# Kernel tuning notes

Hardware: AMD Instinct MI355X
Metric: run time of the kernel (lower is better)

Reference implementation:

```python
import jax, jax.numpy as jnp
import numpy as np

B, N, WIDTH, HEADS = 4, 2048, 1024, 16
HEAD_DIM = WIDTH // HEADS  # 64


def setup_inputs() -> dict:
    key = jax.random.key(0)
    k1, k2, k3 = jax.random.split(key, 3)
    x = jax.random.normal(k1, (B, N, WIDTH), dtype=jnp.float32)
    # Linear weights stored as [in, out] (torch stores [out, in]; math y = x @ W_in_out + b)
    w_qkv = jax.random.normal(k2, (WIDTH, 3 * WIDTH), dtype=jnp.float32) * (1.0 / np.sqrt(WIDTH))
    b_qkv = jnp.zeros((3 * WIDTH,), dtype=jnp.float32)
    w_proj = jax.random.normal(k3, (WIDTH, WIDTH), dtype=jnp.float32) * (1.0 / np.sqrt(WIDTH))
    b_proj = jnp.zeros((WIDTH,), dtype=jnp.float32)
    return {"x": x, "w_qkv": w_qkv, "b_qkv": b_qkv, "w_proj": w_proj, "b_proj": b_proj}


def reference(x, w_qkv, b_qkv, w_proj, b_proj):
    bs, n_ctx, width = x.shape
    qkv = x @ w_qkv + b_qkv                      # [b, n, 3*width]
    attn_ch = HEAD_DIM                            # width // heads
    scale = 1.0 / np.sqrt(np.sqrt(attn_ch))       # 1/sqrt(sqrt(d)) applied to q and k
    qkv = qkv.reshape(bs, n_ctx, HEADS, 3 * attn_ch)
    q, k, v = jnp.split(qkv, 3, axis=-1)          # each [b, n, h, d]
    weight = jnp.einsum('bthc,bshc->bhts', q * scale, k * scale)
    weight = jax.nn.softmax(weight, axis=-1)
    out = jnp.einsum('bhts,bshc->bthc', weight, v).reshape(bs, n_ctx, -1)
    return out @ w_proj + b_proj
```

## Files before the change

kernel.cpp:

```cpp
#include <hip/hip_runtime.h>

typedef __attribute__((ext_vector_type(8))) short bf16x8;
typedef __attribute__((ext_vector_type(4))) float f32x4;
typedef __attribute__((ext_vector_type(8))) unsigned short u16x8;
typedef __attribute__((ext_vector_type(4))) unsigned short u16x4;
typedef __attribute__((ext_vector_type(2))) unsigned u32x2;

__device__ __forceinline__ unsigned short f2bf(float f) {
  unsigned u = __builtin_bit_cast(unsigned, f);
  return (unsigned short)((u + 0x7fffu + ((u >> 16) & 1u)) >> 16);
}

__device__ __forceinline__ unsigned cvt_pk_bf16(float lo, float hi) {
  unsigned r;
  asm("v_cvt_pk_bf16_f32 %0, %1, %2" : "=v"(r) : "v"(lo), "v"(hi));
  return r;
}

__device__ __forceinline__ void gl_lds16(const void* g, void* l) {
  __builtin_amdgcn_global_load_lds((const __attribute__((address_space(1))) unsigned*)g,
                                   (__attribute__((address_space(3))) unsigned*)l, 16, 0, 0);
}

__global__ __launch_bounds__(256) void k_prep(const float* __restrict__ x,
                                              unsigned short* __restrict__ xb,
                                              const float* __restrict__ wq,
                                              unsigned short* __restrict__ wqT,
                                              const float* __restrict__ wp,
                                              unsigned short* __restrict__ wpT) {
  __shared__ float tile[32][33];
  const int bx = blockIdx.x;
  const int t = threadIdx.x;
  if (bx < 4096) {
    const int i = bx * 256 + t;
    const float4* s = (const float4*)x;
    float4 a = s[2 * i], b = s[2 * i + 1];
    u16x8 o;
    o[0] = f2bf(a.x); o[1] = f2bf(a.y); o[2] = f2bf(a.z); o[3] = f2bf(a.w);
    o[4] = f2bf(b.x); o[5] = f2bf(b.y); o[6] = f2bf(b.z); o[7] = f2bf(b.w);
    *(u16x8*)(xb + 8 * (size_t)i) = o;
    return;
  }
  const int b = bx - 4096;
  const float* w;
  unsigned short* wT;
  int Nn, bb;
  if (b < 3072) { w = wq; wT = wqT; Nn = 3072; bb = b; }
  else          { w = wp; wT = wpT; Nn = 1024; bb = b - 3072; }
  const int k0 = (bb & 31) * 32, n0 = (bb >> 5) * 32;
  const int i = t >> 3, j = (t & 7) * 4;
  float4 v = *(const float4*)(w + (size_t)(k0 + i) * Nn + n0 + j);
  tile[i][j] = v.x; tile[i][j + 1] = v.y; tile[i][j + 2] = v.z; tile[i][j + 3] = v.w;
  __syncthreads();
  const int n = i, k4 = j;
  u16x4 o;
  o[0] = f2bf(tile[k4 + 0][n]); o[1] = f2bf(tile[k4 + 1][n]);
  o[2] = f2bf(tile[k4 + 2][n]); o[3] = f2bf(tile[k4 + 3][n]);
  *(u16x4*)(wT + (size_t)(n0 + n) * 1024 + k0 + k4) = o;
}

template <int EPI>
__global__ __launch_bounds__(256) void k_gemm(const unsigned short* __restrict__ A,
                                              const unsigned short* __restrict__ Bt,
                                              const float* __restrict__ bias, int Nx,
                                              float* __restrict__ outF,
                                              unsigned short* __restrict__ Qb,
                                              unsigned short* __restrict__ Kb,
                                              unsigned short* __restrict__ Vb) {
  __shared__ __attribute__((aligned(16))) unsigned short As[3][128 * 32];
  __shared__ __attribute__((aligned(16))) unsigned short Bs[3][128 * 32];
  const int t = threadIdx.x;
  const int jj = blockIdx.x >> 3;
  const int brow = ((blockIdx.x & 7) * 8 + (jj & 7)) * 128;
  const int bcol = (jj >> 3) * 128;
  const int lane = t & 63, wid = t >> 6;
  const int wr = (wid >> 1) * 64, wc = (wid & 1) * 64;
  const int g = lane >> 4, qr = lane & 15;
  const f32x4 fzero = {0.f, 0.f, 0.f, 0.f};
  f32x4 acc[4][4];
#pragma unroll
  for (int i = 0; i < 4; ++i)
#pragma unroll
    for (int n = 0; n < 4; ++n) acc[i][n] = fzero;
  const int srow = t >> 2;
  const int sg = (t & 3) ^ (srow & 3);
  const unsigned short* Ag0 = A + (size_t)(brow + srow) * 1024 + sg * 8;
  const unsigned short* Bg0 = Bt + (size_t)(bcol + srow) * 1024 + sg * 8;

#define STAGE(s_, kt_)                                        \
  do {                                                        \
    const int koff = (kt_) * 32;                              \
    gl_lds16(Ag0 + koff, &As[s_][t * 8]);                     \
    gl_lds16(Ag0 + 64 * 1024 + koff, &As[s_][2048 + t * 8]);  \
    gl_lds16(Bg0 + koff, &Bs[s_][t * 8]);                     \
    gl_lds16(Bg0 + 64 * 1024 + koff, &Bs[s_][2048 + t * 8]);  \
  } while (0)

  STAGE(0, 0);
  STAGE(1, 1);
  for (int kt = 0; kt < 32; ++kt) {
    const int s = kt % 3;
    if (kt < 31) {
      asm volatile("s_waitcnt vmcnt(4)" ::: "memory");
    } else {
      asm volatile("s_waitcnt vmcnt(0)" ::: "memory");
    }
    __builtin_amdgcn_s_barrier();
    __builtin_amdgcn_sched_barrier(0);
    bf16x8 a[4], b[4];
#pragma unroll
    for (int i = 0; i < 4; ++i) {
      const int r = wr + i * 16 + qr;
      a[i] = *(const bf16x8*)&As[s][r * 32 + ((g ^ (r & 3)) << 3)];
    }
#pragma unroll
    for (int n = 0; n < 4; ++n) {
      const int r = wc + n * 16 + qr;
      b[n] = *(const bf16x8*)&Bs[s][r * 32 + ((g ^ (r & 3)) << 3)];
    }
    __builtin_amdgcn_s_setprio(1);
#pragma unroll
    for (int i = 0; i < 4; ++i)
#pragma unroll
      for (int n = 0; n < 4; ++n)
        acc[i][n] = __builtin_amdgcn_mfma_f32_16x16x32_bf16(a[i], b[n], acc[i][n], 0, 0, 0);
    __builtin_amdgcn_s_setprio(0);
    if (kt < 30) STAGE((kt + 2) % 3, kt + 2);
  }
#undef STAGE
#pragma unroll
  for (int i = 0; i < 4; ++i) {
#pragma unroll
    for (int n = 0; n < 4; ++n) {
      const int col = bcol + wc + n * 16 + qr;
      const float bv = bias[col];
      float v4[4];
#pragma unroll
      for (int r = 0; r < 4; ++r) v4[r] = acc[i][n][r] + bv;
      const int row0 = brow + wr + i * 16 + g * 4;
      if constexpr (EPI == 0) {
#pragma unroll
        for (int r = 0; r < 4; ++r) outF[(size_t)(row0 + r) * Nx + col] = v4[r];
      } else {
        const int bb = row0 >> 11, tkn0 = row0 & 2047;
        const unsigned c = (unsigned)col;
        const unsigned h = c / 192u;
        const unsigned rem = c - h * 192u;
        const unsigned which = rem >> 6, d = rem & 63u;
        if (which == 2u) {
          u16x4 pk;
#pragma unroll
          for (int r = 0; r < 4; ++r) pk[r] = f2bf(v4[r]);
          *(u16x4*)&Vb[(size_t)(((unsigned)bb * 16u + h) * 64u + d) * 2048u + (unsigned)tkn0] = pk;
        } else {
          const float sc = (which == 0u) ? (0.35355339059327373f * 1.4426950408889634f)
                                         : 0.35355339059327373f;
          unsigned short* dst = (which == 0u) ? Qb : Kb;
#pragma unroll
          for (int r = 0; r < 4; ++r)
            dst[(size_t)(((unsigned)bb * 16u + h) * 2048u + (unsigned)(tkn0 + r)) * 64u + d] =
                f2bf(v4[r] * sc);
        }
      }
    }
  }
}

__global__ __launch_bounds__(512, 4) void k_attn(const unsigned short* __restrict__ Qb,
                                                 const unsigned short* __restrict__ Kb,
                                                 const unsigned short* __restrict__ Vt,
                                                 unsigned short* __restrict__ Ao) {
  __shared__ __attribute__((aligned(16))) unsigned short Kl[2][64][64];
  __shared__ __attribute__((aligned(16))) unsigned short Vl[2][64][64];
  __shared__ __attribute__((aligned(16))) unsigned short Pl[8][2][16][72];
  const int bid = blockIdx.x;
  const int bh = (bid & 7) * 8 + ((bid >> 3) & 7);
  const int qt = bid >> 6;
  const int t = threadIdx.x, lane = t & 63, w = t >> 6;
  const int g = lane >> 4, q = lane & 15;
  const int q0 = qt * 256 + w * 32;
  const unsigned short* Qbase = Qb + ((size_t)bh * 2048 + q0) * 64;
  const char* Kg = (const char*)(Kb + (size_t)bh * 2048 * 64);
  const char* Vg = (const char*)(Vt + (size_t)bh * 64 * 2048);
  const int lr = lane >> 3, lc = lane & 7;
  const int swz = (lc ^ lr) << 4;
  const char* Ksrc = Kg + (size_t)(8 * w + lr) * 128 + swz;
  const char* Vsrc = Vg + (size_t)(8 * w + lr) * 4096 + swz;
  unsigned short* Kd[2], *Vd[2];
  Kd[0] = &Kl[0][8 * w][0] + lane * 8;
  Kd[1] = &Kl[1][8 * w][0] + lane * 8;
  Vd[0] = &Vl[0][8 * w][0] + lane * 8;
  Vd[1] = &Vl[1][8 * w][0] + lane * 8;

#define STAGE(buf, it_)                              \
  do {                                               \
    gl_lds16(Ksrc + (size_t)(it_) * 8192, Kd[buf]);  \
    gl_lds16(Vsrc + (size_t)(it_) * 128, Vd[buf]);   \
  } while (0)

  bf16x8 qf[2][2];
#pragma unroll
  for (int G = 0; G < 2; ++G)
#pragma unroll
    for (int h = 0; h < 2; ++h)
      qf[G][h] = *(const bf16x8*)(Qbase + (size_t)(G * 16 + q) * 64 + h * 32 + g * 8);
  const f32x4 fzero = {0.f, 0.f, 0.f, 0.f};
  f32x4 o0[4], o1[4];
#pragma unroll
  for (int i = 0; i < 4; ++i) { o0[i] = fzero; o1[i] = fzero; }
  float l0 = 0.f, l1 = 0.f;

  STAGE(0, 0);
  __syncthreads();

  for (int it = 0; it < 32; ++it) {
    const int cur = it & 1;
    if (it < 31) STAGE(cur ^ 1, it + 1);
    f32x4 s0[4], s1[4];
    __builtin_amdgcn_s_setprio(1);
#pragma unroll
    for (int kf = 0; kf < 4; ++kf) {
      const int row = kf * 16 + q;
      const char* kp = (const char*)&Kl[cur][row][0];
      const int sw = (row & 7) << 4;
      bf16x8 kaL = *(const bf16x8*)(kp + ((g * 16) ^ sw));
      bf16x8 kaH = *(const bf16x8*)(kp + ((64 + g * 16) ^ sw));
      s0[kf] = __builtin_amdgcn_mfma_f32_16x16x32_bf16(kaL, qf[0][0], fzero, 0, 0, 0);
      s0[kf] = __builtin_amdgcn_mfma_f32_16x16x32_bf16(kaH, qf[0][1], s0[kf], 0, 0, 0);
      s1[kf] = __builtin_amdgcn_mfma_f32_16x16x32_bf16(kaL, qf[1][0], fzero, 0, 0, 0);
      s1[kf] = __builtin_amdgcn_mfma_f32_16x16x32_bf16(kaH, qf[1][1], s1[kf], 0, 0, 0);
    }
    __builtin_amdgcn_s_setprio(0);
    {
      unsigned short* Pw = &Pl[w][0][q][0];
#pragma unroll
      for (int kf = 0; kf < 4; ++kf) {
        const float e0 = __builtin_amdgcn_exp2f(s0[kf][0]);
        const float e1 = __builtin_amdgcn_exp2f(s0[kf][1]);
        const float e2 = __builtin_amdgcn_exp2f(s0[kf][2]);
        const float e3 = __builtin_amdgcn_exp2f(s0[kf][3]);
        l0 += (e0 + e1) + (e2 + e3);
        u32x2 pk;
        pk[0] = cvt_pk_bf16(e0, e1);
        pk[1] = cvt_pk_bf16(e2, e3);
        *(u32x2*)(Pw + (8 * kf + 2 * g) * 2) = pk;
      }
    }
    {
      unsigned short* Pw = &Pl[w][1][q][0];
#pragma unroll
      for (int kf = 0; kf < 4; ++kf) {
        const float e0 = __builtin_amdgcn_exp2f(s1[kf][0]);
        const float e1 = __builtin_amdgcn_exp2f(s1[kf][1]);
        const float e2 = __builtin_amdgcn_exp2f(s1[kf][2]);
        const float e3 = __builtin_amdgcn_exp2f(s1[kf][3]);
        l1 += (e0 + e1) + (e2 + e3);
        u32x2 pk;
        pk[0] = cvt_pk_bf16(e0, e1);
        pk[1] = cvt_pk_bf16(e2, e3);
        *(u32x2*)(Pw + (8 * kf + 2 * g) * 2) = pk;
      }
    }
    asm volatile("" ::: "memory");
    const bf16x8 pa00 = *(const bf16x8*)&Pl[w][0][q][g * 8];
    const bf16x8 pa01 = *(const bf16x8*)&Pl[w][0][q][32 + g * 8];
    const bf16x8 pa10 = *(const bf16x8*)&Pl[w][1][q][g * 8];
    const bf16x8 pa11 = *(const bf16x8*)&Pl[w][1][q][32 + g * 8];
    __builtin_amdgcn_s_setprio(1);
#pragma unroll
    for (int dblk = 0; dblk < 4; ++dblk) {
      const int row = dblk * 16 + q;
      const char* vp = (const char*)&Vl[cur][row][0];
      const int sw = (row & 7) << 4;
      bf16x8 vL = *(const bf16x8*)(vp + ((g * 16) ^ sw));
      bf16x8 vH = *(const bf16x8*)(vp + ((64 + g * 16) ^ sw));
      o0[dblk] = __builtin_amdgcn_mfma_f32_16x16x32_bf16(vL, pa00, o0[dblk], 0, 0, 0);
      o0[dblk] = __builtin_amdgcn_mfma_f32_16x16x32_bf16(vH, pa01, o0[dblk], 0, 0, 0);
      o1[dblk] = __builtin_amdgcn_mfma_f32_16x16x32_bf16(vL, pa10, o1[dblk], 0, 0, 0);
      o1[dblk] = __builtin_amdgcn_mfma_f32_16x16x32_bf16(vH, pa11, o1[dblk], 0, 0, 0);
    }
    __builtin_amdgcn_s_setprio(0);
    __syncthreads();
  }
#undef STAGE
  l0 += __shfl_xor(l0, 16); l0 += __shfl_xor(l0, 32);
  l1 += __shfl_xor(l1, 16); l1 += __shfl_xor(l1, 32);
  const float li0 = 1.0f / l0, li1 = 1.0f / l1;
  const int bb = bh >> 4, hh = bh & 15;
  {
    unsigned short* ob = Ao + ((size_t)bb * 2048 + q0 + q) * 1024 + hh * 64 + 4 * g;
#pragma unroll
    for (int dblk = 0; dblk < 4; ++dblk) {
      u16x4 pk;
#pragma unroll
      for (int r = 0; r < 4; ++r) pk[r] = f2bf(o0[dblk][r] * li0);
      *(u16x4*)(ob + dblk * 16) = pk;
    }
  }
  {
    unsigned short* ob = Ao + ((size_t)bb * 2048 + q0 + 16 + q) * 1024 + hh * 64 + 4 * g;
#pragma unroll
    for (int dblk = 0; dblk < 4; ++dblk) {
      u16x4 pk;
#pragma unroll
      for (int r = 0; r < 4; ++r) pk[r] = f2bf(o1[dblk][r] * li1);
      *(u16x4*)(ob + dblk * 16) = pk;
    }
  }
}

extern "C" void kernel_launch(void* const* d_in, const int* in_sizes, int n_in,
                              void* d_out, int out_size, void* d_ws, size_t ws_size,
                              hipStream_t stream) {
  const float* x = (const float*)d_in[0];
  const float* w_qkv = (const float*)d_in[1];
  const float* b_qkv = (const float*)d_in[2];
  const float* w_proj = (const float*)d_in[3];
  const float* b_proj = (const float*)d_in[4];
  float* out = (float*)d_out;
  char* ws = (char*)d_ws;
  unsigned short* xb = (unsigned short*)(ws);
  unsigned short* wqkvT = (unsigned short*)(ws + 16777216);
  unsigned short* wprojT = (unsigned short*)(ws + 23068672);
  unsigned short* Qb = (unsigned short*)(ws + 25165824);
  unsigned short* Kb = (unsigned short*)(ws + 41943040);
  unsigned short* Vt = (unsigned short*)(ws + 58720256);
  unsigned short* Ao = xb;

  hipLaunchKernelGGL(k_prep, dim3(8192), dim3(256), 0, stream,
                     x, xb, w_qkv, wqkvT, w_proj, wprojT);
  hipLaunchKernelGGL((k_gemm<1>), dim3(1536), dim3(256), 0, stream,
                     xb, wqkvT, b_qkv, 3072, (float*)nullptr, Qb, Kb, Vt);
  hipLaunchKernelGGL(k_attn, dim3(512), dim3(512), 0, stream, Qb, Kb, Vt, Ao);
  hipLaunchKernelGGL((k_gemm<0>), dim3(512), dim3(256), 0, stream,
                     Ao, wprojT, b_proj, 1024, out,
                     (unsigned short*)nullptr, (unsigned short*)nullptr, (unsigned short*)nullptr);
}
```

Baseline: 178.5 us.

## Triple-buffer K tiles and issue loads after compute with explicit vmcnt waits

Reworks the attention K/V staging pipeline. K now uses three LDS buffers and is prefetched two iterations ahead, while V stays double-buffered. The end-of-iteration __syncthreads is replaced by a single s_waitcnt vmcnt plus s_barrier at the top of each iteration, and the next loads are issued after the PV MFMAs. This is meant to hide more global-load latency and drop one barrier per iteration, at the cost of 8 KB more LDS per block and finer-grained, more fragile wait-count logic.

```diff
diff --git a/kernel.cpp b/kernel.cpp
--- a/kernel.cpp
+++ b/kernel.cpp
@@ -170,7 +170,7 @@
                                                  const unsigned short* __restrict__ Kb,
                                                  const unsigned short* __restrict__ Vt,
                                                  unsigned short* __restrict__ Ao) {
-  __shared__ __attribute__((aligned(16))) unsigned short Kl[2][64][64];
+  __shared__ __attribute__((aligned(16))) unsigned short Kl[3][64][64];
   __shared__ __attribute__((aligned(16))) unsigned short Vl[2][64][64];
   __shared__ __attribute__((aligned(16))) unsigned short Pl[8][2][16][72];
   const int bid = blockIdx.x;
@@ -186,17 +186,9 @@
   const int swz = (lc ^ lr) << 4;
   const char* Ksrc = Kg + (size_t)(8 * w + lr) * 128 + swz;
   const char* Vsrc = Vg + (size_t)(8 * w + lr) * 4096 + swz;
-  unsigned short* Kd[2], *Vd[2];
-  Kd[0] = &Kl[0][8 * w][0] + lane * 8;
-  Kd[1] = &Kl[1][8 * w][0] + lane * 8;
-  Vd[0] = &Vl[0][8 * w][0] + lane * 8;
-  Vd[1] = &Vl[1][8 * w][0] + lane * 8;
-
-#define STAGE(buf, it_)                              \
-  do {                                               \
-    gl_lds16(Ksrc + (size_t)(it_) * 8192, Kd[buf]);  \
-    gl_lds16(Vsrc + (size_t)(it_) * 128, Vd[buf]);   \
-  } while (0)
+
+#define KST(s_, it_) gl_lds16(Ksrc + (size_t)(it_) * 8192, &Kl[s_][8 * w][0] + lane * 8)
+#define VST(b_, it_) gl_lds16(Vsrc + (size_t)(it_) * 128, &Vl[b_][8 * w][0] + lane * 8)
 
   bf16x8 qf[2][2];
 #pragma unroll
@@ -210,18 +202,25 @@
   for (int i = 0; i < 4; ++i) { o0[i] = fzero; o1[i] = fzero; }
   float l0 = 0.f, l1 = 0.f;
 
-  STAGE(0, 0);
-  __syncthreads();
+  KST(0, 0);
+  VST(0, 0);
+  KST(1, 1);
 
   for (int it = 0; it < 32; ++it) {
-    const int cur = it & 1;
-    if (it < 31) STAGE(cur ^ 1, it + 1);
+    const int s = it % 3, vb = it & 1;
+    if (it < 31) {
+      asm volatile("s_waitcnt vmcnt(1)" ::: "memory");
+    } else {
+      asm volatile("s_waitcnt vmcnt(0)" ::: "memory");
+    }
+    __builtin_amdgcn_s_barrier();
+    __builtin_amdgcn_sched_barrier(0);
     f32x4 s0[4], s1[4];
     __builtin_amdgcn_s_setprio(1);
 #pragma unroll
     for (int kf = 0; kf < 4; ++kf) {
       const int row = kf * 16 + q;
-      const char* kp = (const char*)&Kl[cur][row][0];
+      const char* kp = (const char*)&Kl[s][row][0];
       const int sw = (row & 7) << 4;
       bf16x8 kaL = *(const bf16x8*)(kp + ((g * 16) ^ sw));
       bf16x8 kaH = *(const bf16x8*)(kp + ((64 + g * 16) ^ sw));
@@ -270,7 +269,7 @@
 #pragma unroll
     for (int dblk = 0; dblk < 4; ++dblk) {
       const int row = dblk * 16 + q;
-      const char* vp = (const char*)&Vl[cur][row][0];
+      const char* vp = (const char*)&Vl[vb][row][0];
       const int sw = (row & 7) << 4;
       bf16x8 vL = *(const bf16x8*)(vp + ((g * 16) ^ sw));
       bf16x8 vH = *(const bf16x8*)(vp + ((64 + g * 16) ^ sw));
@@ -280,9 +279,11 @@
       o1[dblk] = __builtin_amdgcn_mfma_f32_16x16x32_bf16(vH, pa11, o1[dblk], 0, 0, 0);
     }
     __builtin_amdgcn_s_setprio(0);
-    __syncthreads();
-  }
-#undef STAGE
+    if (it < 31) VST(vb ^ 1, it + 1);
+    if (it < 30) KST((it + 2) % 3, it + 2);
+  }
+#undef KST
+#undef VST
   l0 += __shfl_xor(l0, 16); l0 += __shfl_xor(l0, 32);
   l1 += __shfl_xor(l1, 16); l1 += __shfl_xor(l1, 32);
   const float li0 = 1.0f / l0, li1 = 1.0f / l1;
```

Measured after the change: 177.8 us. No clear change (-0.4%).
